# Optimization experiments

Hardware: AMD Instinct MI355X
Metric: run time of the kernel (lower is better)

## Reference

```python
import jax, jax.numpy as jnp
import numpy as np

N_PTS0 = 32      # n_sampling_points
N_PTS1 = 8       # n_final_points after maxpool
DIM_LOI = 128    # hardcoded via reshape(128, ...) in LinePooling
DIM_FC = 1024
N_LABELS = 3
C_IN = 256
H = W = 128
N_LINES = 16000


def setup_inputs() -> dict:
    key = jax.random.key(0)
    ks = jax.random.split(key, 8)
    features = jax.random.normal(ks[0], (1, C_IN, H, W), jnp.float32)
    # line endpoints (x1,y1,x2,y2) in feature-map coordinates [0, 128)
    lines = jax.random.uniform(ks[1], (N_LINES, 4), jnp.float32) * 128.0
    w_fc1 = jax.random.normal(ks[2], (DIM_LOI, C_IN), jnp.float32) / np.sqrt(C_IN)
    b_fc1 = jnp.zeros((DIM_LOI,), jnp.float32)
    w1 = jax.random.normal(ks[3], (DIM_FC, DIM_LOI * N_PTS1), jnp.float32) / np.sqrt(DIM_LOI * N_PTS1)
    b1 = jnp.zeros((DIM_FC,), jnp.float32)
    w2 = jax.random.normal(ks[4], (DIM_FC, DIM_FC), jnp.float32) / np.sqrt(DIM_FC)
    b2 = jnp.zeros((DIM_FC,), jnp.float32)
    w3 = jax.random.normal(ks[5], (N_LABELS, DIM_FC), jnp.float32) / np.sqrt(DIM_FC)
    b3 = jnp.zeros((N_LABELS,), jnp.float32)
    return {"features": features, "lines": lines, "w_fc1": w_fc1, "b_fc1": b_fc1,
            "w1": w1, "b1": b1, "w2": w2, "b2": b2, "w3": w3, "b3": b3}


def _line_pool(loi, lines):
    # loi: [C, H, W]; lines: [N, 4] -> pooled features [N, C * N_PTS1]
    h, w = loi.shape[1], loi.shape[2]
    tspan = jnp.linspace(0.0, 1.0, N_PTS0)[None, None, :]          # [1,1,S]
    U, V = lines[:, :2], lines[:, 2:]                               # [N,2]
    pts = U[:, :, None] * tspan + V[:, :, None] * (1.0 - tspan) - 0.5  # [N,2,S]
    pts = pts.transpose(0, 2, 1).reshape(-1, 2)                     # [N*S,2]
    px, py = pts[:, 0], pts[:, 1]
    px0 = jnp.clip(jnp.floor(px), 0.0, w - 1)
    py0 = jnp.clip(jnp.floor(py), 0.0, h - 1)
    px1 = jnp.clip(px0 + 1.0, 0.0, w - 1)
    py1 = jnp.clip(py0 + 1.0, 0.0, h - 1)
    px0l, py0l = px0.astype(jnp.int32), py0.astype(jnp.int32)
    px1l, py1l = px1.astype(jnp.int32), py1.astype(jnp.int32)
    # four-corner bilinear gather: each gather is [C, N*S]
    xp = (loi[:, py0l, px0l] * (py1 - py) * (px1 - px)
          + loi[:, py1l, px0l] * (py - py0) * (px1 - px)
          + loi[:, py0l, px1l] * (py1 - py) * (px - px0)
          + loi[:, py1l, px1l] * (py - py0) * (px - px0))
    xp = xp.reshape(DIM_LOI, -1, N_PTS0).transpose(1, 0, 2)         # [N,C,S]
    k = N_PTS0 // N_PTS1
    xp = xp.reshape(xp.shape[0], DIM_LOI, N_PTS1, k).max(axis=-1)   # maxpool1d
    return xp.reshape(-1, N_PTS1 * DIM_LOI)                         # [N, C*P1]


def reference(features, lines, w_fc1, b_fc1, w1, b1, w2, b2, w3, b3):
    # fc1: 1x1 conv 256 -> 128 + ReLU (batch = 1)
    loi = jax.nn.relu(jnp.einsum('oc,chw->ohw', w_fc1, features[0]) + b_fc1[:, None, None])
    feat = _line_pool(loi, lines)                                   # [N, 1024]
    x = jax.nn.relu(feat @ w1.T + b1)
    x = jax.nn.relu(x @ w2.T + b2)
    logits = x @ w3.T + b3                                          # [N, N_LABELS]
    return logits
```

## Files before the change

kernel.cpp:

```cpp
#include <hip/hip_runtime.h>
#include <hip/hip_bf16.h>
#include <math.h>

#define C_IN 256
#define HW 128
#define NPIX (HW*HW)
#define DIM_LOI 128
#define N_LINES 16000
#define N_PTS0 32
#define N_PTS1 8
#define DIM_FC 1024
#define N_LABELS 3

typedef __attribute__((ext_vector_type(8))) short short8;
typedef __attribute__((ext_vector_type(4))) float f32x4;

__global__ __launch_bounds__(256) void prep_kernel(
    const float* __restrict__ feats, __hip_bfloat16* __restrict__ featsT,
    const float* __restrict__ w1,    __hip_bfloat16* __restrict__ w1p,
    const float* __restrict__ w2,    __hip_bfloat16* __restrict__ w2b,
    const float* __restrict__ wfc1,  __hip_bfloat16* __restrict__ wfc1b)
{
    __shared__ float tile[64][65];
    const int b = blockIdx.x;
    const int t = threadIdx.x;

    if (b < 1024) {
        const int p0 = (b & 255) * 64;
        const int c0 = (b >> 8) * 64;
#pragma unroll
        for (int i = 0; i < 4; ++i) {
            int c = (t >> 4) + i * 16;
            int p4 = (t & 15) * 4;
            float4 v = *(const float4*)(feats + (size_t)(c0 + c) * NPIX + p0 + p4);
            tile[c][p4 + 0] = v.x;
            tile[c][p4 + 1] = v.y;
            tile[c][p4 + 2] = v.z;
            tile[c][p4 + 3] = v.w;
        }
        __syncthreads();
#pragma unroll
        for (int i = 0; i < 2; ++i) {
            int p = (t >> 3) + i * 32;
            int cc = (t & 7) * 8;
            union { __hip_bfloat16 h[8]; uint4 u4; } pk;
#pragma unroll
            for (int j = 0; j < 8; ++j) pk.h[j] = __float2bfloat16(tile[cc + j][p]);
            *(uint4*)(featsT + (size_t)(p0 + p) * C_IN + c0 + cc) = pk.u4;
        }
    } else if (b < 2048) {
        float* row = &tile[0][0];
        const int n = b - 1024;
        ((float4*)row)[t] = ((const float4*)(w1 + (size_t)n * 1024))[t];
        __syncthreads();
        unsigned int* dst = (unsigned int*)(w1p + (size_t)n * 1024);
#pragma unroll
        for (int pass = 0; pass < 2; ++pass) {
            int j = pass * 256 + t;
            int k0 = 2 * j, k1 = 2 * j + 1;
            float v0 = row[(k0 & 127) * 8 + (k0 >> 7)];
            float v1 = row[(k1 & 127) * 8 + (k1 >> 7)];
            union { __hip_bfloat16 h[2]; unsigned int u; } pk;
            pk.h[0] = __float2bfloat16(v0);
            pk.h[1] = __float2bfloat16(v1);
            dst[j] = pk.u;
        }
    } else if (b < 3072) {
        int i = (b - 2048) * 256 + t;
        float4 v = *(const float4*)(w2 + (size_t)i * 4);
        union { __hip_bfloat16 h[4]; uint2 u; } pk;
        pk.h[0] = __float2bfloat16(v.x);
        pk.h[1] = __float2bfloat16(v.y);
        pk.h[2] = __float2bfloat16(v.z);
        pk.h[3] = __float2bfloat16(v.w);
        *(uint2*)(w2b + (size_t)i * 4) = pk.u;
    } else {
        int i = (b - 3072) * 256 + t;
        float4 v = *(const float4*)(wfc1 + (size_t)i * 4);
        union { __hip_bfloat16 h[4]; uint2 u; } pk;
        pk.h[0] = __float2bfloat16(v.x);
        pk.h[1] = __float2bfloat16(v.y);
        pk.h[2] = __float2bfloat16(v.z);
        pk.h[3] = __float2bfloat16(v.w);
        *(uint2*)(wfc1b + (size_t)i * 4) = pk.u;
    }
}

__global__ __launch_bounds__(256) void pool_kernel(
    const __hip_bfloat16* __restrict__ loi,
    const float* __restrict__ lines,
    __hip_bfloat16* __restrict__ feat)
{
    __shared__ int   offs[2][N_PTS0][4];
    __shared__ float wts[2][N_PTS0][4];
    const int h     = threadIdx.x >> 7;
    const int lt    = threadIdx.x & 127;
    const int point = lt >> 4;
    const int t16   = lt & 15;
    const int l     = blockIdx.x * 2 + h;

    if (lt < N_PTS0) {
        int j = lt;
        float tt = (float)j * (1.0f / 31.0f);
        float U0 = lines[4 * l + 0], U1 = lines[4 * l + 1];
        float V0 = lines[4 * l + 2], V1 = lines[4 * l + 3];
        float px = U0 * tt + V0 * (1.0f - tt) - 0.5f;
        float py = U1 * tt + V1 * (1.0f - tt) - 0.5f;
        float px0 = fminf(fmaxf(floorf(px), 0.0f), 127.0f);
        float py0 = fminf(fmaxf(floorf(py), 0.0f), 127.0f);
        float px1 = fminf(fmaxf(px0 + 1.0f, 0.0f), 127.0f);
        float py1 = fminf(fmaxf(py0 + 1.0f, 0.0f), 127.0f);
        int ix0 = (int)px0, iy0 = (int)py0, ix1 = (int)px1, iy1 = (int)py1;
        float wx0 = px1 - px, wx1 = px - px0;
        float wy0 = py1 - py, wy1 = py - py0;
        offs[h][j][0] = (iy0 * HW + ix0) * 16;
        offs[h][j][1] = (iy1 * HW + ix0) * 16;
        offs[h][j][2] = (iy0 * HW + ix1) * 16;
        offs[h][j][3] = (iy1 * HW + ix1) * 16;
        wts[h][j][0] = wy0 * wx0;
        wts[h][j][1] = wy1 * wx0;
        wts[h][j][2] = wy0 * wx1;
        wts[h][j][3] = wy1 * wx1;
    }
    __syncthreads();

    const uint4* loi4 = (const uint4*)loi;
    uint4* featw = (uint4*)(feat + (size_t)l * (N_PTS1 * DIM_LOI));

    float b0 = -INFINITY, b1 = -INFINITY, b2 = -INFINITY, b3 = -INFINITY;
    float b4 = -INFINITY, b5 = -INFINITY, b6 = -INFINITY, b7 = -INFINITY;
#pragma unroll
    for (int q = 0; q < 4; ++q) {
        int j = point * 4 + q;
        uint4 v0 = loi4[offs[h][j][0] + t16];
        uint4 v1 = loi4[offs[h][j][1] + t16];
        uint4 v2 = loi4[offs[h][j][2] + t16];
        uint4 v3 = loi4[offs[h][j][3] + t16];
        float w0 = wts[h][j][0], w1 = wts[h][j][1];
        float w2 = wts[h][j][2], w3 = wts[h][j][3];
        float s;
        s = w0 * __uint_as_float(v0.x << 16) + w1 * __uint_as_float(v1.x << 16)
          + w2 * __uint_as_float(v2.x << 16) + w3 * __uint_as_float(v3.x << 16);
        b0 = fmaxf(b0, s);
        s = w0 * __uint_as_float(v0.x & 0xffff0000u) + w1 * __uint_as_float(v1.x & 0xffff0000u)
          + w2 * __uint_as_float(v2.x & 0xffff0000u) + w3 * __uint_as_float(v3.x & 0xffff0000u);
        b1 = fmaxf(b1, s);
        s = w0 * __uint_as_float(v0.y << 16) + w1 * __uint_as_float(v1.y << 16)
          + w2 * __uint_as_float(v2.y << 16) + w3 * __uint_as_float(v3.y << 16);
        b2 = fmaxf(b2, s);
        s = w0 * __uint_as_float(v0.y & 0xffff0000u) + w1 * __uint_as_float(v1.y & 0xffff0000u)
          + w2 * __uint_as_float(v2.y & 0xffff0000u) + w3 * __uint_as_float(v3.y & 0xffff0000u);
        b3 = fmaxf(b3, s);
        s = w0 * __uint_as_float(v0.z << 16) + w1 * __uint_as_float(v1.z << 16)
          + w2 * __uint_as_float(v2.z << 16) + w3 * __uint_as_float(v3.z << 16);
        b4 = fmaxf(b4, s);
        s = w0 * __uint_as_float(v0.z & 0xffff0000u) + w1 * __uint_as_float(v1.z & 0xffff0000u)
          + w2 * __uint_as_float(v2.z & 0xffff0000u) + w3 * __uint_as_float(v3.z & 0xffff0000u);
        b5 = fmaxf(b5, s);
        s = w0 * __uint_as_float(v0.w << 16) + w1 * __uint_as_float(v1.w << 16)
          + w2 * __uint_as_float(v2.w << 16) + w3 * __uint_as_float(v3.w << 16);
        b6 = fmaxf(b6, s);
        s = w0 * __uint_as_float(v0.w & 0xffff0000u) + w1 * __uint_as_float(v1.w & 0xffff0000u)
          + w2 * __uint_as_float(v2.w & 0xffff0000u) + w3 * __uint_as_float(v3.w & 0xffff0000u);
        b7 = fmaxf(b7, s);
    }
    union { __hip_bfloat16 hh[8]; uint4 u; } pk;
    pk.hh[0] = __float2bfloat16(b0);
    pk.hh[1] = __float2bfloat16(b1);
    pk.hh[2] = __float2bfloat16(b2);
    pk.hh[3] = __float2bfloat16(b3);
    pk.hh[4] = __float2bfloat16(b4);
    pk.hh[5] = __float2bfloat16(b5);
    pk.hh[6] = __float2bfloat16(b6);
    pk.hh[7] = __float2bfloat16(b7);
    featw[point * 16 + t16] = pk.u;
}

__global__ __launch_bounds__(256) void mfma_gemm(
    const __hip_bfloat16* __restrict__ A,
    const __hip_bfloat16* __restrict__ B,
    const float* __restrict__ bias,
    __hip_bfloat16* __restrict__ out,
    int M, int N, int K, int n_tiles)
{
    __shared__ __hip_bfloat16 As[2][128 * 64];
    __shared__ __hip_bfloat16 Bs[2][128 * 64];
    const int tid  = threadIdx.x;
    const int lane = tid & 63;
    const int wave = tid >> 6;
    const int wr = wave >> 1, wc = wave & 1;
    const int quad = lane >> 4;
    const int l16  = lane & 15;

    const int lid = blockIdx.x;
    const int per = gridDim.x >> 3;
    const int g   = (lid & 7) * per + (lid >> 3);
    const int n0 = (g % n_tiles) * 128;
    const int m0 = (g / n_tiles) * 128;

    f32x4 acc[4][4];
#pragma unroll
    for (int i = 0; i < 4; ++i)
#pragma unroll
        for (int j = 0; j < 4; ++j) { f32x4 z = {0.f, 0.f, 0.f, 0.f}; acc[i][j] = z; }

    auto stage = [&](int k0, int buf) {
#pragma unroll
        for (int s = 0; s < 4; ++s) {
            int li   = s * 256 + tid;
            int row  = (li & 511) >> 2;
            int ke   = (li >> 9) * 32 + (li & 3) * 8;
            const __hip_bfloat16* ga = A + (size_t)(m0 + row) * K + k0 + ke;
            const __hip_bfloat16* gb = B + (size_t)(n0 + row) * K + k0 + ke;
            int chunk = s * 256 + (tid & ~63);
            __builtin_amdgcn_global_load_lds(
                (const __attribute__((address_space(1))) unsigned int*)ga,
                (__attribute__((address_space(3))) unsigned int*)(As[buf] + chunk * 8),
                16, 0, 0);
            __builtin_amdgcn_global_load_lds(
                (const __attribute__((address_space(1))) unsigned int*)gb,
                (__attribute__((address_space(3))) unsigned int*)(Bs[buf] + chunk * 8),
                16, 0, 0);
        }
    };

    const int nk = K >> 6;
    stage(0, 0);
    __syncthreads();

    for (int kt = 0; kt < nk; ++kt) {
        const int cur = kt & 1;
        if (kt + 1 < nk) stage((kt + 1) << 6, cur ^ 1);

#pragma unroll
        for (int kh = 0; kh < 2; ++kh) {
            const short* ap = (const short*)As[cur] + kh * 4096;
            const short* bp = (const short*)Bs[cur] + kh * 4096;
            short8 af[4], bf[4];
#pragma unroll
            for (int mt = 0; mt < 4; ++mt) {
                int row = wr * 64 + mt * 16 + l16;
                af[mt] = *(const short8*)(ap + row * 32 + quad * 8);
            }
#pragma unroll
            for (int nt = 0; nt < 4; ++nt) {
                int row = wc * 64 + nt * 16 + l16;
                bf[nt] = *(const short8*)(bp + row * 32 + quad * 8);
            }
#pragma unroll
            for (int mt = 0; mt < 4; ++mt)
#pragma unroll
                for (int nt = 0; nt < 4; ++nt)
                    acc[mt][nt] = __builtin_amdgcn_mfma_f32_16x16x32_bf16(
                        af[mt], bf[nt], acc[mt][nt], 0, 0, 0);
        }
        __syncthreads();
    }

#pragma unroll
    for (int nt = 0; nt < 4; ++nt) {
        int n = n0 + wc * 64 + nt * 16 + l16;
        float bv = bias[n];
#pragma unroll
        for (int mt = 0; mt < 4; ++mt) {
            int mbase = m0 + wr * 64 + mt * 16 + quad * 4;
#pragma unroll
            for (int r = 0; r < 4; ++r) {
                float v = acc[mt][nt][r] + bv;
                v = v > 0.0f ? v : 0.0f;
                out[(size_t)(mbase + r) * N + n] = (__hip_bfloat16)v;
            }
        }
    }
}

__global__ __launch_bounds__(256) void head_kernel(
    const __hip_bfloat16* __restrict__ x2,
    const float* __restrict__ w3,
    const float* __restrict__ b3,
    float* __restrict__ out)
{
    const int gtid = blockIdx.x * blockDim.x + threadIdx.x;
    const int l = gtid >> 6;
    const int lane = threadIdx.x & 63;
    if (l >= N_LINES) return;
    const __hip_bfloat16* xr = x2 + (size_t)l * DIM_FC;
    float s0 = 0.0f, s1 = 0.0f, s2 = 0.0f;
#pragma unroll
    for (int it = 0; it < 2; ++it) {
        int k = it * 512 + lane * 8;
        uint4 xv = *(const uint4*)(xr + k);
        float x[8];
        x[0] = __uint_as_float(xv.x << 16);
        x[1] = __uint_as_float(xv.x & 0xffff0000u);
        x[2] = __uint_as_float(xv.y << 16);
        x[3] = __uint_as_float(xv.y & 0xffff0000u);
        x[4] = __uint_as_float(xv.z << 16);
        x[5] = __uint_as_float(xv.z & 0xffff0000u);
        x[6] = __uint_as_float(xv.w << 16);
        x[7] = __uint_as_float(xv.w & 0xffff0000u);
#pragma unroll
        for (int h = 0; h < 2; ++h) {
            int kk = k + h * 4;
            float4 wa = *(const float4*)(w3 + 0 * DIM_FC + kk);
            float4 wb = *(const float4*)(w3 + 1 * DIM_FC + kk);
            float4 wc = *(const float4*)(w3 + 2 * DIM_FC + kk);
            s0 += x[h*4+0] * wa.x + x[h*4+1] * wa.y + x[h*4+2] * wa.z + x[h*4+3] * wa.w;
            s1 += x[h*4+0] * wb.x + x[h*4+1] * wb.y + x[h*4+2] * wb.z + x[h*4+3] * wb.w;
            s2 += x[h*4+0] * wc.x + x[h*4+1] * wc.y + x[h*4+2] * wc.z + x[h*4+3] * wc.w;
        }
    }
#pragma unroll
    for (int off = 32; off > 0; off >>= 1) {
        s0 += __shfl_xor(s0, off);
        s1 += __shfl_xor(s1, off);
        s2 += __shfl_xor(s2, off);
    }
    if (lane == 0) {
        out[(size_t)l * 3 + 0] = s0 + b3[0];
        out[(size_t)l * 3 + 1] = s1 + b3[1];
        out[(size_t)l * 3 + 2] = s2 + b3[2];
    }
}

extern "C" void kernel_launch(void* const* d_in, const int* in_sizes, int n_in,
                              void* d_out, int out_size, void* d_ws, size_t ws_size,
                              hipStream_t stream) {
    const float* features = (const float*)d_in[0];
    const float* lines    = (const float*)d_in[1];
    const float* w_fc1    = (const float*)d_in[2];
    const float* b_fc1    = (const float*)d_in[3];
    const float* w1       = (const float*)d_in[4];
    const float* b1       = (const float*)d_in[5];
    const float* w2       = (const float*)d_in[6];
    const float* b2       = (const float*)d_in[7];
    const float* w3       = (const float*)d_in[8];
    const float* b3       = (const float*)d_in[9];
    float* out = (float*)d_out;

    char* ws = (char*)d_ws;
    __hip_bfloat16* loi    = (__hip_bfloat16*)ws;
    __hip_bfloat16* featb  = (__hip_bfloat16*)(ws + (size_t)8 * 1024 * 1024);
    __hip_bfloat16* x1b    = (__hip_bfloat16*)(ws + (size_t)40 * 1024 * 1024);
    __hip_bfloat16* x2b    = featb;
    __hip_bfloat16* w1b    = (__hip_bfloat16*)(ws + (size_t)72 * 1024 * 1024);
    __hip_bfloat16* w2b    = (__hip_bfloat16*)(ws + (size_t)74 * 1024 * 1024);
    __hip_bfloat16* featsT = (__hip_bfloat16*)(ws + (size_t)76 * 1024 * 1024);
    __hip_bfloat16* wfc1b  = (__hip_bfloat16*)(ws + (size_t)84 * 1024 * 1024);

    prep_kernel<<<dim3(3104), 256, 0, stream>>>(
        features, featsT, w1, w1b, w2, w2b, w_fc1, wfc1b);

    mfma_gemm<<<dim3(NPIX / 128), 256, 0, stream>>>(
        featsT, wfc1b, b_fc1, loi, NPIX, DIM_LOI, C_IN, 1);

    pool_kernel<<<dim3(N_LINES / 2), 256, 0, stream>>>(loi, lines, featb);

    mfma_gemm<<<dim3((N_LINES / 128) * (DIM_FC / 128)), 256, 0, stream>>>(
        featb, w1b, b1, x1b, N_LINES, DIM_FC, DIM_FC, DIM_FC / 128);

    mfma_gemm<<<dim3((N_LINES / 128) * (DIM_FC / 128)), 256, 0, stream>>>(
        x1b, w2b, b2, x2b, N_LINES, DIM_FC, DIM_FC, DIM_FC / 128);

    head_kernel<<<dim3((N_LINES * 64 + 255) / 256), 256, 0, stream>>>(x2b, w3, b3, out);
}
```

Before: 209.9 us.

## Use 256x256-tile pipelined MFMA GEMM with padded line count for FC layers

Adds a new 512-thread GEMM kernel with 256x256 output tiles that stages operands straight into LDS using global_load_lds, with XOR swizzling and a multi-stage software pipeline that interleaves loads, barriers and MFMA phases. The line dimension is padded to 16128 so it divides evenly into 256-row tiles, and the pool kernel zero-fills the padded rows. The goal is more data reuse per tile and better overlap of memory and compute in the two large FC GEMMs. The cost is extra work on the padded rows, higher register and LDS use, and fewer blocks, which can leave some compute units idle.

```diff
diff --git a/kernel.cpp b/kernel.cpp
--- a/kernel.cpp
+++ b/kernel.cpp
@@ -7,6 +7,7 @@
 #define NPIX (HW*HW)
 #define DIM_LOI 128
 #define N_LINES 16000
+#define N_PAD 16128
 #define N_PTS0 32
 #define N_PTS1 8
 #define DIM_FC 1024
@@ -98,6 +99,13 @@
     const int point = lt >> 4;
     const int t16   = lt & 15;
     const int l     = blockIdx.x * 2 + h;
+
+    if (l >= N_LINES) {
+        uint4 z = {0u, 0u, 0u, 0u};
+        uint4* fw = (uint4*)(feat + (size_t)l * (N_PTS1 * DIM_LOI));
+        fw[point * 16 + t16] = z;
+        return;
+    }
 
     if (lt < N_PTS0) {
         int j = lt;
@@ -274,6 +282,250 @@
     }
 }
 
+__global__ __launch_bounds__(512, 2) void mfma_gemm256(
+    const __hip_bfloat16* __restrict__ A,
+    const __hip_bfloat16* __restrict__ B,
+    const float* __restrict__ bias,
+    __hip_bfloat16* __restrict__ out,
+    int M, int N, int K, int n_tiles)
+{
+    __shared__ __align__(16) short smem[65536];
+    const int tid  = threadIdx.x;
+    const int lane = tid & 63;
+    const int wave = tid >> 6;
+    const int wr   = wave >> 2;
+    const int wc   = wave & 3;
+    const int quad = lane >> 4;
+    const int l16  = lane & 15;
+
+    const int g  = blockIdx.x;
+    const int n0 = (g % n_tiles) * 256;
+    const int m0 = (g / n_tiles) * 256;
+
+
+    auto stageHalf = [&](int dstBase, const __hip_bfloat16* G, int rowG0, int k0) {
+#pragma unroll
+        for (int j = 0; j < 2; ++j) {
+            const int c   = j * 512 + tid;
+            const int row = c >> 3;
+            const int kb  = (c & 7) << 4;
+            const int kbl = kb ^ ((row & 3) << 5);
+            const __hip_bfloat16* src = G + (size_t)(rowG0 + row) * K + k0 + (kbl >> 1);
+            const short* dst = smem + dstBase + j * 4096 + (wave << 9);
+            __builtin_amdgcn_global_load_lds(
+                (const __attribute__((address_space(1))) unsigned int*)src,
+                (__attribute__((address_space(3))) unsigned int*)dst, 16, 0, 0);
+        }
+    };
+
+    auto ldA = [&](int buf, int mt, int ks) -> short8 {
+        int r    = ((mt >> 2) << 7) + (wr << 6) + ((mt & 3) << 4) + l16;
+        int koff = ((ks << 6) + (quad << 4)) ^ ((l16 & 3) << 5);
+        return *(const short8*)(smem + buf * 16384 + r * 64 + (koff >> 1));
+    };
+    auto ldB = [&](int buf, int nt, int ks) -> short8 {
+        int r    = (wc << 6) + (nt << 4) + l16;
+        int koff = ((ks << 6) + (quad << 4)) ^ ((l16 & 3) << 5);
+        return *(const short8*)(smem + 32768 + buf * 16384 + r * 64 + (koff >> 1));
+    };
+
+    f32x4 acc[8][4];
+#pragma unroll
+    for (int i = 0; i < 8; ++i)
+#pragma unroll
+        for (int j = 0; j < 4; ++j) { f32x4 z = {0.f, 0.f, 0.f, 0.f}; acc[i][j] = z; }
+
+    short8 af[4][2], b01[2][2], b23[2][2];
+
+    const int NT2 = K >> 7;
+
+    stageHalf(0,                 A, m0,       0);
+    stageHalf(32768,             B, n0,       0);
+    stageHalf(8192,              A, m0 + 128, 0);
+    stageHalf(32768 + 8192,      B, n0 + 128, 0);
+    stageHalf(16384,             A, m0,       64);
+    stageHalf(32768 + 16384,     B, n0,       64);
+    stageHalf(16384 + 8192,      A, m0 + 128, 64);
+    asm volatile("s_waitcnt vmcnt(6)" ::: "memory");
+    __builtin_amdgcn_sched_barrier(0);
+    __builtin_amdgcn_s_barrier();
+
+#pragma unroll 1
+    for (int it = 0; it < NT2; ++it) {
+        const bool more = (it + 1 < NT2);
+        const int kc1 = (2 * it + 1) << 6;
+        const int kn0 = (2 * it + 2) << 6;
+        const int kn1 = (2 * it + 3) << 6;
+
+#pragma unroll
+        for (int mt = 0; mt < 4; ++mt) { af[mt][0] = ldA(0, mt, 0); af[mt][1] = ldA(0, mt, 1); }
+#pragma unroll
+        for (int nt = 0; nt < 2; ++nt) { b01[nt][0] = ldB(0, nt, 0); b01[nt][1] = ldB(0, nt, 1); }
+        stageHalf(32768 + 16384 + 8192, B, n0 + 128, kc1);
+        __builtin_amdgcn_s_barrier();
+        asm volatile("s_waitcnt lgkmcnt(0)" ::: "memory");
+        __builtin_amdgcn_sched_barrier(0);
+        __builtin_amdgcn_s_setprio(1);
+#pragma unroll
+        for (int ks = 0; ks < 2; ++ks)
+#pragma unroll
+            for (int mt = 0; mt < 4; ++mt)
+#pragma unroll
+                for (int nt = 0; nt < 2; ++nt)
+                    acc[mt][nt] = __builtin_amdgcn_mfma_f32_16x16x32_bf16(
+                        af[mt][ks], b01[nt][ks], acc[mt][nt], 0, 0, 0);
+        __builtin_amdgcn_s_setprio(0);
+        __builtin_amdgcn_s_barrier();
+
+#pragma unroll
+        for (int nt = 0; nt < 2; ++nt) { b23[nt][0] = ldB(0, nt + 2, 0); b23[nt][1] = ldB(0, nt + 2, 1); }
+        if (more) stageHalf(0, A, m0, kn0);
+        __builtin_amdgcn_s_barrier();
+        asm volatile("s_waitcnt lgkmcnt(0)" ::: "memory");
+        __builtin_amdgcn_sched_barrier(0);
+        __builtin_amdgcn_s_setprio(1);
+#pragma unroll
+        for (int ks = 0; ks < 2; ++ks)
+#pragma unroll
+            for (int mt = 0; mt < 4; ++mt)
+#pragma unroll
+                for (int nt = 0; nt < 2; ++nt)
+                    acc[mt][nt + 2] = __builtin_amdgcn_mfma_f32_16x16x32_bf16(
+                        af[mt][ks], b23[nt][ks], acc[mt][nt + 2], 0, 0, 0);
+        __builtin_amdgcn_s_setprio(0);
+        __builtin_amdgcn_s_barrier();
+
+#pragma unroll
+        for (int mt = 0; mt < 4; ++mt) { af[mt][0] = ldA(0, mt + 4, 0); af[mt][1] = ldA(0, mt + 4, 1); }
+        if (more) stageHalf(32768, B, n0, kn0);
+        __builtin_amdgcn_s_barrier();
+        asm volatile("s_waitcnt lgkmcnt(0)" ::: "memory");
+        __builtin_amdgcn_sched_barrier(0);
+        __builtin_amdgcn_s_setprio(1);
+#pragma unroll
+        for (int ks = 0; ks < 2; ++ks)
+#pragma unroll
+            for (int mt = 0; mt < 4; ++mt)
+#pragma unroll
+                for (int nt = 0; nt < 2; ++nt)
+                    acc[mt + 4][nt] = __builtin_amdgcn_mfma_f32_16x16x32_bf16(
+                        af[mt][ks], b01[nt][ks], acc[mt + 4][nt], 0, 0, 0);
+        __builtin_amdgcn_s_setprio(0);
+        __builtin_amdgcn_s_barrier();
+
+        if (more) stageHalf(8192, A, m0 + 128, kn0);
+        __builtin_amdgcn_s_barrier();
+        asm volatile("s_waitcnt lgkmcnt(0)" ::: "memory");
+        __builtin_amdgcn_sched_barrier(0);
+        __builtin_amdgcn_s_setprio(1);
+#pragma unroll
+        for (int ks = 0; ks < 2; ++ks)
+#pragma unroll
+            for (int mt = 0; mt < 4; ++mt)
+#pragma unroll
+                for (int nt = 0; nt < 2; ++nt)
+                    acc[mt + 4][nt + 2] = __builtin_amdgcn_mfma_f32_16x16x32_bf16(
+                        af[mt][ks], b23[nt][ks], acc[mt + 4][nt + 2], 0, 0, 0);
+        __builtin_amdgcn_s_setprio(0);
+        if (more) { asm volatile("s_waitcnt vmcnt(6)" ::: "memory"); }
+        else      { asm volatile("s_waitcnt vmcnt(0)" ::: "memory"); }
+        __builtin_amdgcn_sched_barrier(0);
+        __builtin_amdgcn_s_barrier();
+
+#pragma unroll
+        for (int mt = 0; mt < 4; ++mt) { af[mt][0] = ldA(1, mt, 0); af[mt][1] = ldA(1, mt, 1); }
+#pragma unroll
+        for (int nt = 0; nt < 2; ++nt) { b01[nt][0] = ldB(1, nt, 0); b01[nt][1] = ldB(1, nt, 1); }
+        if (more) stageHalf(32768 + 8192, B, n0 + 128, kn0);
+        __builtin_amdgcn_s_barrier();
+        asm volatile("s_waitcnt lgkmcnt(0)" ::: "memory");
+        __builtin_amdgcn_sched_barrier(0);
+        __builtin_amdgcn_s_setprio(1);
+#pragma unroll
+        for (int ks = 0; ks < 2; ++ks)
+#pragma unroll
+            for (int mt = 0; mt < 4; ++mt)
+#pragma unroll
+                for (int nt = 0; nt < 2; ++nt)
+                    acc[mt][nt] = __builtin_amdgcn_mfma_f32_16x16x32_bf16(
+                        af[mt][ks], b01[nt][ks], acc[mt][nt], 0, 0, 0);
+        __builtin_amdgcn_s_setprio(0);
+        __builtin_amdgcn_s_barrier();
+
+#pragma unroll
+        for (int nt = 0; nt < 2; ++nt) { b23[nt][0] = ldB(1, nt + 2, 0); b23[nt][1] = ldB(1, nt + 2, 1); }
+        if (more) stageHalf(16384, A, m0, kn1);
+        __builtin_amdgcn_s_barrier();
+        asm volatile("s_waitcnt lgkmcnt(0)" ::: "memory");
+        __builtin_amdgcn_sched_barrier(0);
+        __builtin_amdgcn_s_setprio(1);
+#pragma unroll
+        for (int ks = 0; ks < 2; ++ks)
+#pragma unroll
+            for (int mt = 0; mt < 4; ++mt)
+#pragma unroll
+                for (int nt = 0; nt < 2; ++nt)
+                    acc[mt][nt + 2] = __builtin_amdgcn_mfma_f32_16x16x32_bf16(
+                        af[mt][ks], b23[nt][ks], acc[mt][nt + 2], 0, 0, 0);
+        __builtin_amdgcn_s_setprio(0);
+        __builtin_amdgcn_s_barrier();
+
+#pragma unroll
+        for (int mt = 0; mt < 4; ++mt) { af[mt][0] = ldA(1, mt + 4, 0); af[mt][1] = ldA(1, mt + 4, 1); }
+        if (more) stageHalf(32768 + 16384, B, n0, kn1);
+        __builtin_amdgcn_s_barrier();
+        asm volatile("s_waitcnt lgkmcnt(0)" ::: "memory");
+        __builtin_amdgcn_sched_barrier(0);
+        __builtin_amdgcn_s_setprio(1);
+#pragma unroll
+        for (int ks = 0; ks < 2; ++ks)
+#pragma unroll
+            for (int mt = 0; mt < 4; ++mt)
+#pragma unroll
+                for (int nt = 0; nt < 2; ++nt)
+                    acc[mt + 4][nt] = __builtin_amdgcn_mfma_f32_16x16x32_bf16(
+                        af[mt][ks], b01[nt][ks], acc[mt + 4][nt], 0, 0, 0);
+        __builtin_amdgcn_s_setprio(0);
+        __builtin_amdgcn_s_barrier();
+
+        if (more) stageHalf(16384 + 8192, A, m0 + 128, kn1);
+        __builtin_amdgcn_s_barrier();
+        asm volatile("s_waitcnt lgkmcnt(0)" ::: "memory");
+        __builtin_amdgcn_sched_barrier(0);
+        __builtin_amdgcn_s_setprio(1);
+#pragma unroll
+        for (int ks = 0; ks < 2; ++ks)
+#pragma unroll
+            for (int mt = 0; mt < 4; ++mt)
+#pragma unroll
+                for (int nt = 0; nt < 2; ++nt)
+                    acc[mt + 4][nt + 2] = __builtin_amdgcn_mfma_f32_16x16x32_bf16(
+                        af[mt][ks], b23[nt][ks], acc[mt + 4][nt + 2], 0, 0, 0);
+        __builtin_amdgcn_s_setprio(0);
+        if (more) {
+            asm volatile("s_waitcnt vmcnt(6)" ::: "memory");
+            __builtin_amdgcn_sched_barrier(0);
+        }
+        __builtin_amdgcn_s_barrier();
+    }
+
+#pragma unroll
+    for (int nt = 0; nt < 4; ++nt) {
+        int n = n0 + (wc << 6) + (nt << 4) + l16;
+        float bv = bias[n];
+#pragma unroll
+        for (int mt = 0; mt < 8; ++mt) {
+            int mbase = m0 + ((mt >> 2) << 7) + (wr << 6) + ((mt & 3) << 4) + (quad << 2);
+#pragma unroll
+            for (int r = 0; r < 4; ++r) {
+                float v = acc[mt][nt][r] + bv;
+                v = v > 0.0f ? v : 0.0f;
+                out[(size_t)(mbase + r) * N + n] = (__hip_bfloat16)v;
+            }
+        }
+    }
+}
+
 __global__ __launch_bounds__(256) void head_kernel(
     const __hip_bfloat16* __restrict__ x2,
     const float* __restrict__ w3,
@@ -354,13 +606,13 @@
     mfma_gemm<<<dim3(NPIX / 128), 256, 0, stream>>>(
         featsT, wfc1b, b_fc1, loi, NPIX, DIM_LOI, C_IN, 1);
 
-    pool_kernel<<<dim3(N_LINES / 2), 256, 0, stream>>>(loi, lines, featb);
-
-    mfma_gemm<<<dim3((N_LINES / 128) * (DIM_FC / 128)), 256, 0, stream>>>(
-        featb, w1b, b1, x1b, N_LINES, DIM_FC, DIM_FC, DIM_FC / 128);
-
-    mfma_gemm<<<dim3((N_LINES / 128) * (DIM_FC / 128)), 256, 0, stream>>>(
-        x1b, w2b, b2, x2b, N_LINES, DIM_FC, DIM_FC, DIM_FC / 128);
+    pool_kernel<<<dim3(N_PAD / 2), 256, 0, stream>>>(loi, lines, featb);
+
+    mfma_gemm256<<<dim3((N_PAD / 256) * (DIM_FC / 256)), 512, 0, stream>>>(
+        featb, w1b, b1, x1b, N_PAD, DIM_FC, DIM_FC, DIM_FC / 256);
+
+    mfma_gemm256<<<dim3((N_PAD / 256) * (DIM_FC / 256)), 512, 0, stream>>>(
+        x1b, w2b, b2, x2b, N_PAD, DIM_FC, DIM_FC, DIM_FC / 256);
 
     head_kernel<<<dim3((N_LINES * 64 + 255) / 256), 256, 0, stream>>>(x2b, w3, b3, out);
 }
```

After: 208.5 us. No clear change (-0.7%).

## Use 256x256 pipelined MFMA GEMM and fuse final head into second GEMM

Applied to the files above, without the earlier changes.

Replaces the 128-tile GEMMs for the two large FC layers with a 256x256-tile, 512-thread kernel. It uses direct global-to-LDS loads, swizzled shared memory, a double-buffered K pipeline, XCD-aware tile remapping and an LDS-staged coalesced epilogue. Line count is padded to 16128 (pool kernel zero-fills the extra rows) so M divides the tile. The w3 head is fused into the second GEMM's epilogue, writing per-N-block partial logits that a small kernel sums, which avoids writing and re-reading x2. This adds padding work, extra workspace and a more complex schedule with many barriers.

```diff
diff --git a/kernel.cpp b/kernel.cpp
--- a/kernel.cpp
+++ b/kernel.cpp
@@ -7,6 +7,7 @@
 #define NPIX (HW*HW)
 #define DIM_LOI 128
 #define N_LINES 16000
+#define N_PAD 16128
 #define N_PTS0 32
 #define N_PTS1 8
 #define DIM_FC 1024
@@ -98,6 +99,13 @@
     const int point = lt >> 4;
     const int t16   = lt & 15;
     const int l     = blockIdx.x * 2 + h;
+
+    if (l >= N_LINES) {
+        uint4 z = {0u, 0u, 0u, 0u};
+        uint4* fw = (uint4*)(feat + (size_t)l * (N_PTS1 * DIM_LOI));
+        fw[point * 16 + t16] = z;
+        return;
+    }
 
     if (lt < N_PTS0) {
         int j = lt;
@@ -274,53 +282,337 @@
     }
 }
 
-__global__ __launch_bounds__(256) void head_kernel(
-    const __hip_bfloat16* __restrict__ x2,
+#define GEMM256_PROLOG_AND_KLOOP                                              \
+    const int tid  = threadIdx.x;                                             \
+    const int lane = tid & 63;                                                \
+    const int wave = tid >> 6;                                                \
+    const int wr   = wave >> 2;                                               \
+    const int wc   = wave & 3;                                                \
+    const int quad = lane >> 4;                                               \
+    const int l16  = lane & 15;                                               \
+    const int nwg = gridDim.x;                                                \
+    const int q8  = nwg >> 3, r8 = nwg & 7;                                   \
+    const int xcd = blockIdx.x & 7;                                           \
+    const int gb  = (xcd < r8) ? xcd * (q8 + 1) : r8 * (q8 + 1) + (xcd - r8) * q8; \
+    const int g   = gb + (blockIdx.x >> 3);                                   \
+    const int n0 = (g % n_tiles) * 256;                                       \
+    const int m0 = (g / n_tiles) * 256;                                       \
+    auto stageHalf = [&](int dstBase, const __hip_bfloat16* G, int rowG0, int k0) { \
+        _Pragma("unroll")                                                     \
+        for (int j = 0; j < 2; ++j) {                                         \
+            const int c   = j * 512 + tid;                                    \
+            const int row = c >> 3;                                           \
+            const int kb  = (c & 7) << 4;                                     \
+            const int kbl = kb ^ ((row & 7) << 4);                            \
+            const __hip_bfloat16* src = G + (size_t)(rowG0 + row) * K + k0 + (kbl >> 1); \
+            const short* dst = smem + dstBase + j * 4096 + (wave << 9);       \
+            __builtin_amdgcn_global_load_lds(                                 \
+                (const __attribute__((address_space(1))) unsigned int*)src,   \
+                (__attribute__((address_space(3))) unsigned int*)dst, 16, 0, 0); \
+        }                                                                     \
+    };                                                                        \
+    auto ldA = [&](int buf, int mt, int ks) -> short8 {                       \
+        int r    = ((mt >> 2) << 7) + (wr << 6) + ((mt & 3) << 4) + l16;      \
+        int koff = ((ks << 6) + (quad << 4)) ^ ((l16 & 7) << 4);              \
+        return *(const short8*)(smem + buf * 16384 + r * 64 + (koff >> 1));   \
+    };                                                                        \
+    auto ldB = [&](int buf, int nt, int ks) -> short8 {                       \
+        int r    = (wc << 6) + (nt << 4) + l16;                               \
+        int koff = ((ks << 6) + (quad << 4)) ^ ((l16 & 7) << 4);              \
+        return *(const short8*)(smem + 32768 + buf * 16384 + r * 64 + (koff >> 1)); \
+    };                                                                        \
+    f32x4 acc[8][4];                                                          \
+    _Pragma("unroll")                                                         \
+    for (int i = 0; i < 8; ++i)                                               \
+        _Pragma("unroll")                                                     \
+        for (int j = 0; j < 4; ++j) { f32x4 z = {0.f, 0.f, 0.f, 0.f}; acc[i][j] = z; } \
+    short8 af[4][2], b01[2][2], b23[2][2];                                    \
+    const int NT2 = K >> 7;                                                   \
+    stageHalf(0,                 A, m0,       0);                             \
+    stageHalf(32768,             B, n0,       0);                             \
+    stageHalf(8192,              A, m0 + 128, 0);                             \
+    stageHalf(32768 + 8192,      B, n0 + 128, 0);                             \
+    stageHalf(16384,             A, m0,       64);                            \
+    stageHalf(32768 + 16384,     B, n0,       64);                            \
+    stageHalf(16384 + 8192,      A, m0 + 128, 64);                            \
+    asm volatile("s_waitcnt vmcnt(6)" ::: "memory");                          \
+    __builtin_amdgcn_sched_barrier(0);                                        \
+    __builtin_amdgcn_s_barrier();                                             \
+    _Pragma("unroll 1")                                                       \
+    for (int it = 0; it < NT2; ++it) {                                        \
+        const bool more = (it + 1 < NT2);                                     \
+        const int kc1 = (2 * it + 1) << 6;                                    \
+        const int kn0 = (2 * it + 2) << 6;                                    \
+        const int kn1 = (2 * it + 3) << 6;                                    \
+                                                                      \
+        _Pragma("unroll")                                                     \
+        for (int mt = 0; mt < 4; ++mt) { af[mt][0] = ldA(0, mt, 0); af[mt][1] = ldA(0, mt, 1); } \
+        _Pragma("unroll")                                                     \
+        for (int nt = 0; nt < 2; ++nt) { b01[nt][0] = ldB(0, nt, 0); b01[nt][1] = ldB(0, nt, 1); } \
+        stageHalf(32768 + 16384 + 8192, B, n0 + 128, kc1);                    \
+        __builtin_amdgcn_s_barrier();                                         \
+        asm volatile("s_waitcnt lgkmcnt(0)" ::: "memory");                    \
+        __builtin_amdgcn_sched_barrier(0);                                    \
+        __builtin_amdgcn_s_setprio(1);                                        \
+        _Pragma("unroll")                                                     \
+        for (int ks = 0; ks < 2; ++ks)                                        \
+            _Pragma("unroll")                                                 \
+            for (int mt = 0; mt < 4; ++mt)                                    \
+                _Pragma("unroll")                                             \
+                for (int nt = 0; nt < 2; ++nt)                                \
+                    acc[mt][nt] = __builtin_amdgcn_mfma_f32_16x16x32_bf16(    \
+                        af[mt][ks], b01[nt][ks], acc[mt][nt], 0, 0, 0);       \
+        __builtin_amdgcn_s_setprio(0);                                        \
+        __builtin_amdgcn_s_barrier();                                         \
+                                                                      \
+        _Pragma("unroll")                                                     \
+        for (int nt = 0; nt < 2; ++nt) { b23[nt][0] = ldB(0, nt + 2, 0); b23[nt][1] = ldB(0, nt + 2, 1); } \
+        if (more) stageHalf(0, A, m0, kn0);                                   \
+        __builtin_amdgcn_s_barrier();                                         \
+        asm volatile("s_waitcnt lgkmcnt(0)" ::: "memory");                    \
+        __builtin_amdgcn_sched_barrier(0);                                    \
+        __builtin_amdgcn_s_setprio(1);                                        \
+        _Pragma("unroll")                                                     \
+        for (int ks = 0; ks < 2; ++ks)                                        \
+            _Pragma("unroll")                                                 \
+            for (int mt = 0; mt < 4; ++mt)                                    \
+                _Pragma("unroll")                                             \
+                for (int nt = 0; nt < 2; ++nt)                                \
+                    acc[mt][nt + 2] = __builtin_amdgcn_mfma_f32_16x16x32_bf16( \
+                        af[mt][ks], b23[nt][ks], acc[mt][nt + 2], 0, 0, 0);   \
+        __builtin_amdgcn_s_setprio(0);                                        \
+        __builtin_amdgcn_s_barrier();                                         \
+                                                                      \
+        _Pragma("unroll")                                                     \
+        for (int mt = 0; mt < 4; ++mt) { af[mt][0] = ldA(0, mt + 4, 0); af[mt][1] = ldA(0, mt + 4, 1); } \
+        if (more) stageHalf(32768, B, n0, kn0);                               \
+        __builtin_amdgcn_s_barrier();                                         \
+        asm volatile("s_waitcnt lgkmcnt(0)" ::: "memory");                    \
+        __builtin_amdgcn_sched_barrier(0);                                    \
+        __builtin_amdgcn_s_setprio(1);                                        \
+        _Pragma("unroll")                                                     \
+        for (int ks = 0; ks < 2; ++ks)                                        \
+            _Pragma("unroll")                                                 \
+            for (int mt = 0; mt < 4; ++mt)                                    \
+                _Pragma("unroll")                                             \
+                for (int nt = 0; nt < 2; ++nt)                                \
+                    acc[mt + 4][nt] = __builtin_amdgcn_mfma_f32_16x16x32_bf16( \
+                        af[mt][ks], b01[nt][ks], acc[mt + 4][nt], 0, 0, 0);   \
+        __builtin_amdgcn_s_setprio(0);                                        \
+        __builtin_amdgcn_s_barrier();                                         \
+                                                                      \
+        if (more) stageHalf(8192, A, m0 + 128, kn0);                          \
+        __builtin_amdgcn_s_barrier();                                         \
+        asm volatile("s_waitcnt lgkmcnt(0)" ::: "memory");                    \
+        __builtin_amdgcn_sched_barrier(0);                                    \
+        __builtin_amdgcn_s_setprio(1);                                        \
+        _Pragma("unroll")                                                     \
+        for (int ks = 0; ks < 2; ++ks)                                        \
+            _Pragma("unroll")                                                 \
+            for (int mt = 0; mt < 4; ++mt)                                    \
+                _Pragma("unroll")                                             \
+                for (int nt = 0; nt < 2; ++nt)                                \
+                    acc[mt + 4][nt + 2] = __builtin_amdgcn_mfma_f32_16x16x32_bf16( \
+                        af[mt][ks], b23[nt][ks], acc[mt + 4][nt + 2], 0, 0, 0); \
+        __builtin_amdgcn_s_setprio(0);                                        \
+        if (more) { asm volatile("s_waitcnt vmcnt(6)" ::: "memory"); }        \
+        else      { asm volatile("s_waitcnt vmcnt(0)" ::: "memory"); }        \
+        __builtin_amdgcn_sched_barrier(0);                                    \
+        __builtin_amdgcn_s_barrier();                                         \
+                                                                      \
+        _Pragma("unroll")                                                     \
+        for (int mt = 0; mt < 4; ++mt) { af[mt][0] = ldA(1, mt, 0); af[mt][1] = ldA(1, mt, 1); } \
+        _Pragma("unroll")                                                     \
+        for (int nt = 0; nt < 2; ++nt) { b01[nt][0] = ldB(1, nt, 0); b01[nt][1] = ldB(1, nt, 1); } \
+        if (more) stageHalf(32768 + 8192, B, n0 + 128, kn0);                  \
+        __builtin_amdgcn_s_barrier();                                         \
+        asm volatile("s_waitcnt lgkmcnt(0)" ::: "memory");                    \
+        __builtin_amdgcn_sched_barrier(0);                                    \
+        __builtin_amdgcn_s_setprio(1);                                        \
+        _Pragma("unroll")                                                     \
+        for (int ks = 0; ks < 2; ++ks)                                        \
+            _Pragma("unroll")                                                 \
+            for (int mt = 0; mt < 4; ++mt)                                    \
+                _Pragma("unroll")                                             \
+                for (int nt = 0; nt < 2; ++nt)                                \
+                    acc[mt][nt] = __builtin_amdgcn_mfma_f32_16x16x32_bf16(    \
+                        af[mt][ks], b01[nt][ks], acc[mt][nt], 0, 0, 0);       \
+        __builtin_amdgcn_s_setprio(0);                                        \
+        __builtin_amdgcn_s_barrier();                                         \
+                                                                      \
+        _Pragma("unroll")                                                     \
+        for (int nt = 0; nt < 2; ++nt) { b23[nt][0] = ldB(1, nt + 2, 0); b23[nt][1] = ldB(1, nt + 2, 1); } \
+        if (more) stageHalf(16384, A, m0, kn1);                               \
+        __builtin_amdgcn_s_barrier();                                         \
+        asm volatile("s_waitcnt lgkmcnt(0)" ::: "memory");                    \
+        __builtin_amdgcn_sched_barrier(0);                                    \
+        __builtin_amdgcn_s_setprio(1);                                        \
+        _Pragma("unroll")                                                     \
+        for (int ks = 0; ks < 2; ++ks)                                        \
+            _Pragma("unroll")                                                 \
+            for (int mt = 0; mt < 4; ++mt)                                    \
+                _Pragma("unroll")                                             \
+                for (int nt = 0; nt < 2; ++nt)                                \
+                    acc[mt][nt + 2] = __builtin_amdgcn_mfma_f32_16x16x32_bf16( \
+                        af[mt][ks], b23[nt][ks], acc[mt][nt + 2], 0, 0, 0);   \
+        __builtin_amdgcn_s_setprio(0);                                        \
+        __builtin_amdgcn_s_barrier();                                         \
+                                                                      \
+        _Pragma("unroll")                                                     \
+        for (int mt = 0; mt < 4; ++mt) { af[mt][0] = ldA(1, mt + 4, 0); af[mt][1] = ldA(1, mt + 4, 1); } \
+        if (more) stageHalf(32768 + 16384, B, n0, kn1);                       \
+        __builtin_amdgcn_s_barrier();                                         \
+        asm volatile("s_waitcnt lgkmcnt(0)" ::: "memory");                    \
+        __builtin_amdgcn_sched_barrier(0);                                    \
+        __builtin_amdgcn_s_setprio(1);                                        \
+        _Pragma("unroll")                                                     \
+        for (int ks = 0; ks < 2; ++ks)                                        \
+            _Pragma("unroll")                                                 \
+            for (int mt = 0; mt < 4; ++mt)                                    \
+                _Pragma("unroll")                                             \
+                for (int nt = 0; nt < 2; ++nt)                                \
+                    acc[mt + 4][nt] = __builtin_amdgcn_mfma_f32_16x16x32_bf16( \
+                        af[mt][ks], b01[nt][ks], acc[mt + 4][nt], 0, 0, 0);   \
+        __builtin_amdgcn_s_setprio(0);                                        \
+        __builtin_amdgcn_s_barrier();                                         \
+                                                                      \
+        if (more) stageHalf(16384 + 8192, A, m0 + 128, kn1);                  \
+        __builtin_amdgcn_s_barrier();                                         \
+        asm volatile("s_waitcnt lgkmcnt(0)" ::: "memory");                    \
+        __builtin_amdgcn_sched_barrier(0);                                    \
+        __builtin_amdgcn_s_setprio(1);                                        \
+        _Pragma("unroll")                                                     \
+        for (int ks = 0; ks < 2; ++ks)                                        \
+            _Pragma("unroll")                                                 \
+            for (int mt = 0; mt < 4; ++mt)                                    \
+                _Pragma("unroll")                                             \
+                for (int nt = 0; nt < 2; ++nt)                                \
+                    acc[mt + 4][nt + 2] = __builtin_amdgcn_mfma_f32_16x16x32_bf16( \
+                        af[mt][ks], b23[nt][ks], acc[mt + 4][nt + 2], 0, 0, 0); \
+        __builtin_amdgcn_s_setprio(0);                                        \
+        if (more) {                                                           \
+            asm volatile("s_waitcnt vmcnt(6)" ::: "memory");                  \
+            __builtin_amdgcn_sched_barrier(0);                                \
+        }                                                                     \
+        __builtin_amdgcn_s_barrier();                                         \
+    }
+
+__global__ __launch_bounds__(512, 2) void mfma_gemm256(
+    const __hip_bfloat16* __restrict__ A,
+    const __hip_bfloat16* __restrict__ B,
+    const float* __restrict__ bias,
+    __hip_bfloat16* __restrict__ out,
+    int M, int N, int K, int n_tiles)
+{
+    __shared__ __align__(16) short smem[65536];
+    GEMM256_PROLOG_AND_KLOOP
+
+    __syncthreads();
+#pragma unroll
+    for (int nt = 0; nt < 4; ++nt) {
+        int ncol = (wc << 6) + (nt << 4) + l16;
+        float bv = bias[n0 + ncol];
+#pragma unroll
+        for (int mt = 0; mt < 8; ++mt) {
+            int rbase = ((mt >> 2) << 7) + (wr << 6) + ((mt & 3) << 4) + (quad << 2);
+#pragma unroll
+            for (int r = 0; r < 4; ++r) {
+                float v = acc[mt][nt][r] + bv;
+                v = v > 0.0f ? v : 0.0f;
+                int row = rbase + r;
+                int chunk = (ncol >> 3) ^ (row & 7);
+                union { __hip_bfloat16 h; short s; } cv;
+                cv.h = (__hip_bfloat16)v;
+                smem[row * 256 + chunk * 8 + (ncol & 7)] = cv.s;
+            }
+        }
+    }
+    __syncthreads();
+#pragma unroll
+    for (int p = 0; p < 16; ++p) {
+        int ci  = p * 512 + tid;
+        int row = ci >> 5;
+        int cg  = ci & 31;
+        short8 vv = *(const short8*)(smem + row * 256 + ((cg ^ (row & 7)) << 3));
+        *(short8*)(out + (size_t)(m0 + row) * N + n0 + cg * 8) = vv;
+    }
+}
+
+__global__ __launch_bounds__(512, 2) void mfma_gemm256_head(
+    const __hip_bfloat16* __restrict__ A,
+    const __hip_bfloat16* __restrict__ B,
+    const float* __restrict__ bias,
     const float* __restrict__ w3,
+    float* __restrict__ pl,
+    int M, int N, int K, int n_tiles)
+{
+    __shared__ __align__(16) short smem[65536];
+    GEMM256_PROLOG_AND_KLOOP
+
+    const int nblk = n0 >> 8;
+    float w3v[3][4];
+    float bv[4];
+#pragma unroll
+    for (int nt = 0; nt < 4; ++nt) {
+        int n = n0 + (wc << 6) + (nt << 4) + l16;
+        bv[nt] = bias[n];
+#pragma unroll
+        for (int lbl = 0; lbl < 3; ++lbl) w3v[lbl][nt] = w3[lbl * DIM_FC + n];
+    }
+
+    float* scratch = (float*)smem;
+#pragma unroll
+    for (int mt = 0; mt < 8; ++mt) {
+        int rbase = ((mt >> 2) << 7) + (wr << 6) + ((mt & 3) << 4) + (quad << 2);
+#pragma unroll
+        for (int r = 0; r < 4; ++r) {
+            float s0 = 0.f, s1 = 0.f, s2 = 0.f;
+#pragma unroll
+            for (int nt = 0; nt < 4; ++nt) {
+                float v = acc[mt][nt][r] + bv[nt];
+                v = v > 0.0f ? v : 0.0f;
+                s0 += v * w3v[0][nt];
+                s1 += v * w3v[1][nt];
+                s2 += v * w3v[2][nt];
+            }
+#pragma unroll
+            for (int off = 1; off < 16; off <<= 1) {
+                s0 += __shfl_xor(s0, off);
+                s1 += __shfl_xor(s1, off);
+                s2 += __shfl_xor(s2, off);
+            }
+            if (l16 == 0) {
+                int row = rbase + r;
+                scratch[row * 12 + 0 * 4 + wc] = s0;
+                scratch[row * 12 + 1 * 4 + wc] = s1;
+                scratch[row * 12 + 2 * 4 + wc] = s2;
+            }
+        }
+    }
+    __syncthreads();
+    if (tid < 256) {
+        const float* sr = scratch + tid * 12;
+        float t0 = sr[0] + sr[1] + sr[2]  + sr[3];
+        float t1 = sr[4] + sr[5] + sr[6]  + sr[7];
+        float t2 = sr[8] + sr[9] + sr[10] + sr[11];
+        float* dst = pl + (size_t)nblk * (N_PAD * 3) + (size_t)(m0 + tid) * 3;
+        dst[0] = t0; dst[1] = t1; dst[2] = t2;
+    }
+}
+
+__global__ __launch_bounds__(256) void head_sum(
+    const float* __restrict__ pl,
     const float* __restrict__ b3,
     float* __restrict__ out)
 {
-    const int gtid = blockIdx.x * blockDim.x + threadIdx.x;
-    const int l = gtid >> 6;
-    const int lane = threadIdx.x & 63;
-    if (l >= N_LINES) return;
-    const __hip_bfloat16* xr = x2 + (size_t)l * DIM_FC;
-    float s0 = 0.0f, s1 = 0.0f, s2 = 0.0f;
-#pragma unroll
-    for (int it = 0; it < 2; ++it) {
-        int k = it * 512 + lane * 8;
-        uint4 xv = *(const uint4*)(xr + k);
-        float x[8];
-        x[0] = __uint_as_float(xv.x << 16);
-        x[1] = __uint_as_float(xv.x & 0xffff0000u);
-        x[2] = __uint_as_float(xv.y << 16);
-        x[3] = __uint_as_float(xv.y & 0xffff0000u);
-        x[4] = __uint_as_float(xv.z << 16);
-        x[5] = __uint_as_float(xv.z & 0xffff0000u);
-        x[6] = __uint_as_float(xv.w << 16);
-        x[7] = __uint_as_float(xv.w & 0xffff0000u);
-#pragma unroll
-        for (int h = 0; h < 2; ++h) {
-            int kk = k + h * 4;
-            float4 wa = *(const float4*)(w3 + 0 * DIM_FC + kk);
-            float4 wb = *(const float4*)(w3 + 1 * DIM_FC + kk);
-            float4 wc = *(const float4*)(w3 + 2 * DIM_FC + kk);
-            s0 += x[h*4+0] * wa.x + x[h*4+1] * wa.y + x[h*4+2] * wa.z + x[h*4+3] * wa.w;
-            s1 += x[h*4+0] * wb.x + x[h*4+1] * wb.y + x[h*4+2] * wb.z + x[h*4+3] * wb.w;
-            s2 += x[h*4+0] * wc.x + x[h*4+1] * wc.y + x[h*4+2] * wc.z + x[h*4+3] * wc.w;
-        }
-    }
-#pragma unroll
-    for (int off = 32; off > 0; off >>= 1) {
-        s0 += __shfl_xor(s0, off);
-        s1 += __shfl_xor(s1, off);
-        s2 += __shfl_xor(s2, off);
-    }
-    if (lane == 0) {
-        out[(size_t)l * 3 + 0] = s0 + b3[0];
-        out[(size_t)l * 3 + 1] = s1 + b3[1];
-        out[(size_t)l * 3 + 2] = s2 + b3[2];
-    }
+    int i = blockIdx.x * 256 + threadIdx.x;
+    if (i >= N_LINES * 3) return;
+    float s = b3[i % 3]
+            + pl[0 * (N_PAD * 3) + i]
+            + pl[1 * (N_PAD * 3) + i]
+            + pl[2 * (N_PAD * 3) + i]
+            + pl[3 * (N_PAD * 3) + i];
+    out[i] = s;
 }
 
 extern "C" void kernel_launch(void* const* d_in, const int* in_sizes, int n_in,
@@ -342,11 +634,11 @@
     __hip_bfloat16* loi    = (__hip_bfloat16*)ws;
     __hip_bfloat16* featb  = (__hip_bfloat16*)(ws + (size_t)8 * 1024 * 1024);
     __hip_bfloat16* x1b    = (__hip_bfloat16*)(ws + (size_t)40 * 1024 * 1024);
-    __hip_bfloat16* x2b    = featb;
     __hip_bfloat16* w1b    = (__hip_bfloat16*)(ws + (size_t)72 * 1024 * 1024);
     __hip_bfloat16* w2b    = (__hip_bfloat16*)(ws + (size_t)74 * 1024 * 1024);
     __hip_bfloat16* featsT = (__hip_bfloat16*)(ws + (size_t)76 * 1024 * 1024);
     __hip_bfloat16* wfc1b  = (__hip_bfloat16*)(ws + (size_t)84 * 1024 * 1024);
+    float*          plbuf  = (float*)(ws + (size_t)86 * 1024 * 1024);
 
     prep_kernel<<<dim3(3104), 256, 0, stream>>>(
         features, featsT, w1, w1b, w2, w2b, w_fc1, wfc1b);
@@ -354,13 +646,13 @@
     mfma_gemm<<<dim3(NPIX / 128), 256, 0, stream>>>(
         featsT, wfc1b, b_fc1, loi, NPIX, DIM_LOI, C_IN, 1);
 
-    pool_kernel<<<dim3(N_LINES / 2), 256, 0, stream>>>(loi, lines, featb);
-
-    mfma_gemm<<<dim3((N_LINES / 128) * (DIM_FC / 128)), 256, 0, stream>>>(
-        featb, w1b, b1, x1b, N_LINES, DIM_FC, DIM_FC, DIM_FC / 128);
-
-    mfma_gemm<<<dim3((N_LINES / 128) * (DIM_FC / 128)), 256, 0, stream>>>(
-        x1b, w2b, b2, x2b, N_LINES, DIM_FC, DIM_FC, DIM_FC / 128);
-
-    head_kernel<<<dim3((N_LINES * 64 + 255) / 256), 256, 0, stream>>>(x2b, w3, b3, out);
+    pool_kernel<<<dim3(N_PAD / 2), 256, 0, stream>>>(loi, lines, featb);
+
+    mfma_gemm256<<<dim3((N_PAD / 256) * (DIM_FC / 256)), 512, 0, stream>>>(
+        featb, w1b, b1, x1b, N_PAD, DIM_FC, DIM_FC, DIM_FC / 256);
+
+    mfma_gemm256_head<<<dim3((N_PAD / 256) * (DIM_FC / 256)), 512, 0, stream>>>(
+        x1b, w2b, b2, w3, plbuf, N_PAD, DIM_FC, DIM_FC, DIM_FC / 256);
+
+    head_sum<<<dim3((N_LINES * 3 + 255) / 256), 256, 0, stream>>>(plbuf, b3, out);
 }
```

Measured after the change: 188.4 us. 10.3% less time.
